# Kernel tuning notes

Hardware: AMD Instinct MI355X
Metric: run time of the kernel (lower is better)

The kernel has to match this reference:

```python
import jax, jax.numpy as jnp
import numpy as np

NEG = -1000000000.0
EPS = 1e-05

def setup_inputs() -> dict:
    key = jax.random.key(0)
    k1, k2, k3, k4, k5 = jax.random.split(key, 5)
    B, L, E, Q = 64, 2048, 512, 256
    encoded_vecs = jax.random.normal(k1, (B, L, E), dtype=jnp.float32)
    query = jax.random.normal(k2, (B, Q), dtype=jnp.float32)
    length = jax.random.randint(k3, (B,), 1, L + 1, dtype=jnp.int32)
    # Xavier-normal-ish params
    W1 = jax.random.normal(k4, (E + Q, E), dtype=jnp.float32) * jnp.sqrt(2.0 / (E + Q + E))
    b1 = jnp.zeros((E,), dtype=jnp.float32)
    v = jax.random.normal(k5, (E,), dtype=jnp.float32) * jnp.sqrt(2.0 / (E + 1))
    return {"encoded_vecs": encoded_vecs, "query": query, "length": length,
            "W1": W1, "b1": b1, "v": v}

def reference(encoded_vecs, query, length, W1, b1, v):
    B, L, E = encoded_vecs.shape
    # broadcast 2D query over the length dim (repeat in torch code)
    q = jnp.broadcast_to(query[:, None, :], (B, L, query.shape[-1]))
    h = jnp.concatenate([encoded_vecs, q], axis=2)            # [B, L, E+Q]
    u = jnp.tanh(jnp.einsum('blc,ce->ble', h, W1) + b1)       # [B, L, E]
    logits = jnp.einsum('ble,e->bl', u, v)                    # [B, L]
    # masked softmax (faithful to masked_softmax in source)
    mask = (jnp.arange(L)[None, :] < length[:, None])         # [B, L] bool
    masked_logits = jnp.where(mask, logits, NEG)
    max_logits = jnp.max(masked_logits, axis=1, keepdims=True)
    exps = jnp.exp(masked_logits - max_logits) * mask.astype(logits.dtype)
    attention = exps / (jnp.sum(exps, axis=1, keepdims=True) + EPS)  # [B, L]
    context = jnp.einsum('bl,ble->be', attention, encoded_vecs)      # [B, E]
    return (context, attention)
```

## Files before the change

### kernel.cpp

```cpp
#include <hip/hip_runtime.h>

typedef __attribute__((ext_vector_type(4))) float float4v;
typedef __attribute__((ext_vector_type(2))) float float2v;
typedef __attribute__((ext_vector_type(8))) short short8;
typedef __attribute__((ext_vector_type(4))) float f32x4;
typedef __attribute__((ext_vector_type(4))) int int4v;

#define NEGV (-1000000000.0f)

#define MTOT (64 * 2048)

__device__ __forceinline__ unsigned short f2bf(float f) {
    unsigned int u = __float_as_uint(f);
    u += 0x7fffu + ((u >> 16) & 1u);
    return (unsigned short)(u >> 16);
}

__device__ __forceinline__ void gload_lds16(const void* g, void* l) {
    __builtin_amdgcn_global_load_lds(
        (__attribute__((address_space(1))) unsigned int*)(unsigned long long)(g),
        (__attribute__((address_space(3))) unsigned int*)(unsigned int)(unsigned long long)(l),
        16, 0, 0);
}

__global__ __launch_bounds__(256)
void prep_wt_kernel(const float* __restrict__ W1, unsigned short* __restrict__ Wt) {
    __shared__ float t[32][33];
    int bx = blockIdx.x & 15;
    int by = blockIdx.x >> 4;
    int tx = threadIdx.x & 31;
    int ty = threadIdx.x >> 5;
    #pragma unroll
    for (int i = 0; i < 4; ++i)
        t[ty + 8 * i][tx] = W1[(bx * 32 + ty + 8 * i) * 512 + by * 32 + tx];
    __syncthreads();
    #pragma unroll
    for (int i = 0; i < 4; ++i)
        Wt[(by * 32 + ty + 8 * i) * 512 + bx * 32 + tx] = f2bf(t[tx][ty + 8 * i]);
}

__global__ void prep_qc_kernel(const float* __restrict__ query, const float* __restrict__ W1,
                               const float* __restrict__ b1, float* __restrict__ qc) {
    int b = blockIdx.x;
    int e = threadIdx.x;
    float acc0 = b1[e];
    float acc1 = b1[e + 256];
    const float* w = W1 + 512 * 512;
    #pragma unroll 8
    for (int q = 0; q < 256; ++q) {
        float qv = query[b * 256 + q];
        acc0 += qv * w[q * 512 + e];
        acc1 += qv * w[q * 512 + e + 256];
    }
    qc[b * 512 + e] = acc0;
    qc[b * 512 + e + 256] = acc1;
}

__global__ __launch_bounds__(256, 3)
void gemm_logits_kernel(const float* __restrict__ A,
                        const unsigned short* __restrict__ Wt,
                        const float* __restrict__ qc,
                        const float* __restrict__ v,
                        const int* __restrict__ length,
                        float* __restrict__ part)
{
    int bid = blockIdx.x;
    int x = bid & 7;
    int j = bid >> 3;
    int bm = (j >> 2) * 8 + x;
    int bn = j & 3;
    int b = bm >> 4;
    int l0 = (bm & 15) * 128;
    if (l0 >= length[b]) return;

    __shared__ unsigned short As[3 * 128 * 32];
    __shared__ unsigned short Bs[3 * 128 * 32];

    int tid = threadIdx.x;
    int lane = tid & 63;
    int w = tid >> 6;
    int wm = w >> 1, wn = w & 1;
    long row0 = (long)bm * 128;
    int col0 = bn * 128;

    int ar_r = w * 32 + (lane >> 1);
    int ar_h = lane & 1;
    const char* gAr = (const char*)A + (row0 + ar_r) * 2048 + ar_h * 64;
    int asw = ((ar_r >> 1) & 3) << 4;
    int awr0 = ar_r * 64 + ((ar_h * 32) ^ asw);
    int awr1 = ar_r * 64 + ((ar_h * 32 + 16) ^ asw);

    const char* gB0;
    const char* gB1;
    {
        int off = (w * 2 + 0) * 1024 + lane * 16;
        int r = off >> 6;
        gB0 = (const char*)Wt + (long)(col0 + r) * 1024 + ((off & 63) ^ (((r >> 1) & 3) << 4));
        off = (w * 2 + 1) * 1024 + lane * 16;
        r = off >> 6;
        gB1 = (const char*)Wt + (long)(col0 + r) * 1024 + ((off & 63) ^ (((r >> 1) & 3) << 4));
    }

    int aoff[4], boff[4];
    int kb = 16 * (lane >> 4);
    #pragma unroll
    for (int mi = 0; mi < 4; ++mi) {
        int ar = wm * 64 + (lane & 15) + mi * 16;
        aoff[mi] = ar * 64 + (kb ^ (((ar >> 1) & 3) << 4));
    }
    #pragma unroll
    for (int ni = 0; ni < 4; ++ni) {
        int br = wn * 64 + (lane & 15) + ni * 16;
        boff[ni] = br * 64 + (kb ^ (((br >> 1) & 3) << 4));
    }

    f32x4 acc[4][4] = {};
    float4v P0, P1, P2, P3, Q0, Q1, Q2, Q3;

#define GISSUE(t, R0, R1, R2, R3, sI) do {                                   \
    const char* ga_ = gAr + (t) * 128;                                       \
    R0 = *(const float4v*)(ga_);                                             \
    R1 = *(const float4v*)(ga_ + 16);                                        \
    R2 = *(const float4v*)(ga_ + 32);                                        \
    R3 = *(const float4v*)(ga_ + 48);                                        \
    char* lb_ = (char*)Bs + (sI) * 8192 + w * 2048;                          \
    gload_lds16(gB0 + (t) * 64, lb_);                                        \
    gload_lds16(gB1 + (t) * 64, lb_ + 1024);                                 \
} while (0)

#define CVTW(R0, R1, R2, R3, sW) do {                                        \
    union { int4v i; short8 s; } u0_, u1_;                                   \
    asm("v_cvt_pk_bf16_f32 %0, %1, %2" : "=v"(u0_.i.x) : "v"(R0[0]), "v"(R0[1])); \
    asm("v_cvt_pk_bf16_f32 %0, %1, %2" : "=v"(u0_.i.y) : "v"(R0[2]), "v"(R0[3])); \
    asm("v_cvt_pk_bf16_f32 %0, %1, %2" : "=v"(u0_.i.z) : "v"(R1[0]), "v"(R1[1])); \
    asm("v_cvt_pk_bf16_f32 %0, %1, %2" : "=v"(u0_.i.w) : "v"(R1[2]), "v"(R1[3])); \
    asm("v_cvt_pk_bf16_f32 %0, %1, %2" : "=v"(u1_.i.x) : "v"(R2[0]), "v"(R2[1])); \
    asm("v_cvt_pk_bf16_f32 %0, %1, %2" : "=v"(u1_.i.y) : "v"(R2[2]), "v"(R2[3])); \
    asm("v_cvt_pk_bf16_f32 %0, %1, %2" : "=v"(u1_.i.z) : "v"(R3[0]), "v"(R3[1])); \
    asm("v_cvt_pk_bf16_f32 %0, %1, %2" : "=v"(u1_.i.w) : "v"(R3[2]), "v"(R3[3])); \
    char* aw_ = (char*)As + (sW) * 8192;                                     \
    *(short8*)(aw_ + awr0) = u0_.s;                                          \
    *(short8*)(aw_ + awr1) = u1_.s;                                          \
} while (0)

#define KCOMP(sC) do {                                                       \
    const char* as_ = (const char*)As + (sC) * 8192;                         \
    const char* bs_ = (const char*)Bs + (sC) * 8192;                         \
    short8 af_[4], bf_[4];                                                   \
    _Pragma("unroll")                                                        \
    for (int mi = 0; mi < 4; ++mi) af_[mi] = *(const short8*)(as_ + aoff[mi]); \
    _Pragma("unroll")                                                        \
    for (int ni = 0; ni < 4; ++ni) bf_[ni] = *(const short8*)(bs_ + boff[ni]); \
    _Pragma("unroll")                                                        \
    for (int mi = 0; mi < 4; ++mi)                                           \
        _Pragma("unroll")                                                    \
        for (int ni = 0; ni < 4; ++ni)                                       \
            acc[mi][ni] = __builtin_amdgcn_mfma_f32_16x16x32_bf16(af_[mi], bf_[ni], acc[mi][ni], 0, 0, 0); \
} while (0)

#define KITER(t, L0, L1, L2, L3, C0, C1, C2, C3, sC, sW, sI, ISS, VM) do {   \
    if (ISS) GISSUE((t) + 2, L0, L1, L2, L3, sI);                            \
    KCOMP(sC);                                                               \
    asm volatile("s_waitcnt vmcnt(" #VM ")" ::: "memory");                   \
    CVTW(C0, C1, C2, C3, sW);                                                \
    asm volatile("s_waitcnt lgkmcnt(0)" ::: "memory");                       \
    __builtin_amdgcn_s_barrier();                                            \
    asm volatile("" ::: "memory");                                           \
} while (0)

    GISSUE(0, P0, P1, P2, P3, 0);
    GISSUE(1, Q0, Q1, Q2, Q3, 1);
    asm volatile("s_waitcnt vmcnt(6)" ::: "memory");
    CVTW(P0, P1, P2, P3, 0);
    asm volatile("s_waitcnt lgkmcnt(0)" ::: "memory");
    __builtin_amdgcn_s_barrier();
    asm volatile("" ::: "memory");

    KITER(0,  P0,P1,P2,P3, Q0,Q1,Q2,Q3, 0,1,2, 1, 6);
    KITER(1,  Q0,Q1,Q2,Q3, P0,P1,P2,P3, 1,2,0, 1, 6);
    KITER(2,  P0,P1,P2,P3, Q0,Q1,Q2,Q3, 2,0,1, 1, 6);
    KITER(3,  Q0,Q1,Q2,Q3, P0,P1,P2,P3, 0,1,2, 1, 6);
    KITER(4,  P0,P1,P2,P3, Q0,Q1,Q2,Q3, 1,2,0, 1, 6);
    KITER(5,  Q0,Q1,Q2,Q3, P0,P1,P2,P3, 2,0,1, 1, 6);
    KITER(6,  P0,P1,P2,P3, Q0,Q1,Q2,Q3, 0,1,2, 1, 6);
    KITER(7,  Q0,Q1,Q2,Q3, P0,P1,P2,P3, 1,2,0, 1, 6);
    KITER(8,  P0,P1,P2,P3, Q0,Q1,Q2,Q3, 2,0,1, 1, 6);
    KITER(9,  Q0,Q1,Q2,Q3, P0,P1,P2,P3, 0,1,2, 1, 6);
    KITER(10, P0,P1,P2,P3, Q0,Q1,Q2,Q3, 1,2,0, 1, 6);
    KITER(11, Q0,Q1,Q2,Q3, P0,P1,P2,P3, 2,0,1, 1, 6);
    KITER(12, P0,P1,P2,P3, Q0,Q1,Q2,Q3, 0,1,2, 1, 6);
    KITER(13, Q0,Q1,Q2,Q3, P0,P1,P2,P3, 1,2,0, 1, 6);
    KITER(14, P0,P1,P2,P3, Q0,Q1,Q2,Q3, 2,0,1, 0, 0);
    KCOMP(0);

    const float* qcb = qc + b * 512;
    float vcol[4], qcol[4];
    #pragma unroll
    for (int ni = 0; ni < 4; ++ni) {
        int c = col0 + wn * 64 + ni * 16 + (lane & 15);
        vcol[ni] = v[c];
        qcol[ni] = qcb[c];
    }
    float* pslice = part + (bn * 2 + wn) * MTOT + row0;
    int rbase = wm * 64 + 4 * (lane >> 4);
    #pragma unroll
    for (int mi = 0; mi < 4; ++mi) {
        #pragma unroll
        for (int j2 = 0; j2 < 4; ++j2) {
            float s = 0.f;
            #pragma unroll
            for (int ni = 0; ni < 4; ++ni) {
                float xx = acc[mi][ni][j2] + qcol[ni];
                float e2 = __expf(2.0f * xx);
                float tt = 1.0f - 2.0f * __builtin_amdgcn_rcpf(e2 + 1.0f);
                s += tt * vcol[ni];
            }
            s += __shfl_xor(s, 1);
            s += __shfl_xor(s, 2);
            s += __shfl_xor(s, 4);
            s += __shfl_xor(s, 8);
            if ((lane & 15) == 0)
                pslice[rbase + mi * 16 + j2] = s;
        }
    }
}

__global__ void softmax_kernel(const float* __restrict__ part, const int* __restrict__ length,
                               float* __restrict__ att, float* __restrict__ ctx) {
    int b = blockIdx.x;
    int len = length[b];
    int tid = threadIdx.x;
    int lane = tid & 63, wv = tid >> 6;
    const float* p0 = part + b * 2048;
    float* ab = att + b * 2048;

    ctx[b * 512 + tid] = 0.f;
    ctx[b * 512 + 256 + tid] = 0.f;

    float vals[8];
    float mymax = -3.402823466e38f;
    #pragma unroll
    for (int i = 0; i < 8; ++i) {
        int l = tid + i * 256;
        float xv = NEGV;
        if (l < len) {
            xv = 0.f;
            #pragma unroll
            for (int s = 0; s < 8; ++s)
                xv += p0[s * MTOT + l];
        }
        vals[i] = xv;
        mymax = fmaxf(mymax, xv);
    }
    #pragma unroll
    for (int m = 32; m; m >>= 1) mymax = fmaxf(mymax, __shfl_xor(mymax, m));
    __shared__ float sm[4];
    if (lane == 0) sm[wv] = mymax;
    __syncthreads();
    float bmax = fmaxf(fmaxf(sm[0], sm[1]), fmaxf(sm[2], sm[3]));

    float mysum = 0.f;
    #pragma unroll
    for (int i = 0; i < 8; ++i) {
        int l = tid + i * 256;
        float e = (l < len) ? __expf(vals[i] - bmax) : 0.f;
        vals[i] = e;
        mysum += e;
    }
    #pragma unroll
    for (int m = 32; m; m >>= 1) mysum += __shfl_xor(mysum, m);
    __shared__ float ss[4];
    if (lane == 0) ss[wv] = mysum;
    __syncthreads();
    float tot = ss[0] + ss[1] + ss[2] + ss[3];
    float inv = 1.0f / (tot + 1e-5f);
    #pragma unroll
    for (int i = 0; i < 8; ++i) {
        int l = tid + i * 256;
        ab[l] = vals[i] * inv;
    }
}

__global__ void ctx_kernel(const float* __restrict__ att, const float* __restrict__ enc,
                           const int* __restrict__ length, float* __restrict__ ctx) {
    int b = blockIdx.x;
    int lc = blockIdx.y;
    int len = length[b];
    int l0 = lc * 128;
    if (l0 >= len) return;
    int lim = len - l0;
    if (lim > 128) lim = 128;

    int t = threadIdx.x;
    const float* ab = att + b * 2048 + l0;
    const float* eb = enc + ((long)(b * 2048 + l0)) * 512 + t * 2;
    float c0 = 0.f, c1 = 0.f;
    #pragma unroll 4
    for (int l = 0; l < lim; ++l) {
        float a = ab[l];
        float2v e = *(const float2v*)(eb);
        eb += 512;
        c0 += a * e.x;
        c1 += a * e.y;
    }
    atomicAdd(&ctx[b * 512 + 2 * t], c0);
    atomicAdd(&ctx[b * 512 + 2 * t + 1], c1);
}

extern "C" void kernel_launch(void* const* d_in, const int* in_sizes, int n_in,
                              void* d_out, int out_size, void* d_ws, size_t ws_size,
                              hipStream_t stream) {
    const float* enc    = (const float*)d_in[0];
    const float* query  = (const float*)d_in[1];
    const int*   length = (const int*)d_in[2];
    const float* W1     = (const float*)d_in[3];
    const float* b1     = (const float*)d_in[4];
    const float* v      = (const float*)d_in[5];

    float* out = (float*)d_out;
    float* ctx = out;
    float* att = out + 64 * 512;

    char* ws = (char*)d_ws;
    float* part        = (float*)ws;
    float* qc          = (float*)(ws + 8 * MTOT * 4);
    unsigned short* Wt = (unsigned short*)(ws + 8 * MTOT * 4 + 64 * 512 * 4);

    prep_wt_kernel<<<256, 256, 0, stream>>>(W1, Wt);
    prep_qc_kernel<<<64, 256, 0, stream>>>(query, W1, b1, qc);

    gemm_logits_kernel<<<4096, 256, 0, stream>>>(enc, Wt, qc, v, length, part);

    softmax_kernel<<<64, 256, 0, stream>>>(part, length, att, ctx);

    dim3 g3(64, 16);
    ctx_kernel<<<g3, 256, 0, stream>>>(att, enc, length, ctx);
}
```

Baseline: 145.0 us.

## Widen GEMM tile to 128x256 with 512 threads and reduce partial logits in LDS

The logits GEMM now uses 512-thread blocks covering 256 output columns, so each A tile is loaded and converted to bf16 once per two column halves instead of once per four. The pipeline drops from triple to double buffering with a single prefetch stage, which adds full vmcnt(0) waits at every barrier. Per-wave partial logit sums are reduced in shared memory before being written, which cuts the partial buffer from 8 slices to 2 and lightens the softmax read. The tradeoff is less latency hiding, since each step now waits on its loads, and lower occupancy from the larger blocks.

```diff
diff --git a/kernel.cpp b/kernel.cpp
--- a/kernel.cpp
+++ b/kernel.cpp
@@ -56,7 +56,7 @@
     qc[b * 512 + e + 256] = acc1;
 }
 
-__global__ __launch_bounds__(256, 3)
+__global__ __launch_bounds__(512)
 void gemm_logits_kernel(const float* __restrict__ A,
                         const unsigned short* __restrict__ Wt,
                         const float* __restrict__ qc,
@@ -67,38 +67,38 @@
     int bid = blockIdx.x;
     int x = bid & 7;
     int j = bid >> 3;
-    int bm = (j >> 2) * 8 + x;
-    int bn = j & 3;
+    int bm = (j >> 1) * 8 + x;
+    int bn = j & 1;
     int b = bm >> 4;
     int l0 = (bm & 15) * 128;
     if (l0 >= length[b]) return;
 
-    __shared__ unsigned short As[3 * 128 * 32];
-    __shared__ unsigned short Bs[3 * 128 * 32];
+    __shared__ unsigned short As[2 * 128 * 32];
+    __shared__ unsigned short Bs[2 * 256 * 32];
+    __shared__ float lred[128][4];
 
     int tid = threadIdx.x;
     int lane = tid & 63;
     int w = tid >> 6;
-    int wm = w >> 1, wn = w & 1;
+    int wm = w >> 2, wn = w & 3;
     long row0 = (long)bm * 128;
-    int col0 = bn * 128;
-
-    int ar_r = w * 32 + (lane >> 1);
-    int ar_h = lane & 1;
-    const char* gAr = (const char*)A + (row0 + ar_r) * 2048 + ar_h * 64;
-    int asw = ((ar_r >> 1) & 3) << 4;
-    int awr0 = ar_r * 64 + ((ar_h * 32) ^ asw);
-    int awr1 = ar_r * 64 + ((ar_h * 32 + 16) ^ asw);
-
+    int col0 = bn * 256;
+
+    int ar_r = tid >> 2;
+    int ar_q = tid & 3;
+    const char* gAr = (const char*)A + (row0 + ar_r) * 2048 + ar_q * 32;
+    int awr = ar_r * 64 + ((ar_q * 16) ^ (((ar_r >> 1) & 3) << 4));
+
+    int offw = w * 2048 + lane * 16;
     const char* gB0;
     const char* gB1;
     {
-        int off = (w * 2 + 0) * 1024 + lane * 16;
-        int r = off >> 6;
-        gB0 = (const char*)Wt + (long)(col0 + r) * 1024 + ((off & 63) ^ (((r >> 1) & 3) << 4));
-        off = (w * 2 + 1) * 1024 + lane * 16;
-        r = off >> 6;
-        gB1 = (const char*)Wt + (long)(col0 + r) * 1024 + ((off & 63) ^ (((r >> 1) & 3) << 4));
+        int o = offw;
+        int r = o >> 6;
+        gB0 = (const char*)Wt + (long)(col0 + r) * 1024 + ((o & 63) ^ (((r >> 1) & 3) << 4));
+        o = offw + 1024;
+        r = o >> 6;
+        gB1 = (const char*)Wt + (long)(col0 + r) * 1024 + ((o & 63) ^ (((r >> 1) & 3) << 4));
     }
 
     int aoff[4], boff[4];
@@ -115,83 +115,63 @@
     }
 
     f32x4 acc[4][4] = {};
-    float4v P0, P1, P2, P3, Q0, Q1, Q2, Q3;
-
-#define GISSUE(t, R0, R1, R2, R3, sI) do {                                   \
+    float4v P0, P1;
+
+#define GISSUE(t, sI) do {                                                   \
     const char* ga_ = gAr + (t) * 128;                                       \
-    R0 = *(const float4v*)(ga_);                                             \
-    R1 = *(const float4v*)(ga_ + 16);                                        \
-    R2 = *(const float4v*)(ga_ + 32);                                        \
-    R3 = *(const float4v*)(ga_ + 48);                                        \
-    char* lb_ = (char*)Bs + (sI) * 8192 + w * 2048;                          \
+    P0 = *(const float4v*)(ga_);                                             \
+    P1 = *(const float4v*)(ga_ + 16);                                        \
+    char* lb_ = (char*)Bs + (sI) * 16384 + offw;                             \
     gload_lds16(gB0 + (t) * 64, lb_);                                        \
     gload_lds16(gB1 + (t) * 64, lb_ + 1024);                                 \
 } while (0)
 
-#define CVTW(R0, R1, R2, R3, sW) do {                                        \
-    union { int4v i; short8 s; } u0_, u1_;                                   \
-    asm("v_cvt_pk_bf16_f32 %0, %1, %2" : "=v"(u0_.i.x) : "v"(R0[0]), "v"(R0[1])); \
-    asm("v_cvt_pk_bf16_f32 %0, %1, %2" : "=v"(u0_.i.y) : "v"(R0[2]), "v"(R0[3])); \
-    asm("v_cvt_pk_bf16_f32 %0, %1, %2" : "=v"(u0_.i.z) : "v"(R1[0]), "v"(R1[1])); \
-    asm("v_cvt_pk_bf16_f32 %0, %1, %2" : "=v"(u0_.i.w) : "v"(R1[2]), "v"(R1[3])); \
-    asm("v_cvt_pk_bf16_f32 %0, %1, %2" : "=v"(u1_.i.x) : "v"(R2[0]), "v"(R2[1])); \
-    asm("v_cvt_pk_bf16_f32 %0, %1, %2" : "=v"(u1_.i.y) : "v"(R2[2]), "v"(R2[3])); \
-    asm("v_cvt_pk_bf16_f32 %0, %1, %2" : "=v"(u1_.i.z) : "v"(R3[0]), "v"(R3[1])); \
-    asm("v_cvt_pk_bf16_f32 %0, %1, %2" : "=v"(u1_.i.w) : "v"(R3[2]), "v"(R3[3])); \
-    char* aw_ = (char*)As + (sW) * 8192;                                     \
-    *(short8*)(aw_ + awr0) = u0_.s;                                          \
-    *(short8*)(aw_ + awr1) = u1_.s;                                          \
+#define CVTW(sW) do {                                                        \
+    union { int4v i; short8 s; } u_;                                         \
+    asm("v_cvt_pk_bf16_f32 %0, %1, %2" : "=v"(u_.i.x) : "v"(P0[0]), "v"(P0[1])); \
+    asm("v_cvt_pk_bf16_f32 %0, %1, %2" : "=v"(u_.i.y) : "v"(P0[2]), "v"(P0[3])); \
+    asm("v_cvt_pk_bf16_f32 %0, %1, %2" : "=v"(u_.i.z) : "v"(P1[0]), "v"(P1[1])); \
+    asm("v_cvt_pk_bf16_f32 %0, %1, %2" : "=v"(u_.i.w) : "v"(P1[2]), "v"(P1[3])); \
+    *(short8*)((char*)As + (sW) * 8192 + awr) = u_.s;                        \
 } while (0)
 
 #define KCOMP(sC) do {                                                       \
     const char* as_ = (const char*)As + (sC) * 8192;                         \
-    const char* bs_ = (const char*)Bs + (sC) * 8192;                         \
-    short8 af_[4], bf_[4];                                                   \
+    const char* bs_ = (const char*)Bs + (sC) * 16384;                        \
+    short8 af_[4];                                                           \
     _Pragma("unroll")                                                        \
     for (int mi = 0; mi < 4; ++mi) af_[mi] = *(const short8*)(as_ + aoff[mi]); \
     _Pragma("unroll")                                                        \
-    for (int ni = 0; ni < 4; ++ni) bf_[ni] = *(const short8*)(bs_ + boff[ni]); \
-    _Pragma("unroll")                                                        \
-    for (int mi = 0; mi < 4; ++mi)                                           \
+    for (int ni = 0; ni < 4; ++ni) {                                         \
+        short8 bf_ = *(const short8*)(bs_ + boff[ni]);                       \
         _Pragma("unroll")                                                    \
-        for (int ni = 0; ni < 4; ++ni)                                       \
-            acc[mi][ni] = __builtin_amdgcn_mfma_f32_16x16x32_bf16(af_[mi], bf_[ni], acc[mi][ni], 0, 0, 0); \
+        for (int mi = 0; mi < 4; ++mi)                                       \
+            acc[mi][ni] = __builtin_amdgcn_mfma_f32_16x16x32_bf16(af_[mi], bf_, acc[mi][ni], 0, 0, 0); \
+    }                                                                        \
 } while (0)
 
-#define KITER(t, L0, L1, L2, L3, C0, C1, C2, C3, sC, sW, sI, ISS, VM) do {   \
-    if (ISS) GISSUE((t) + 2, L0, L1, L2, L3, sI);                            \
-    KCOMP(sC);                                                               \
-    asm volatile("s_waitcnt vmcnt(" #VM ")" ::: "memory");                   \
-    CVTW(C0, C1, C2, C3, sW);                                                \
-    asm volatile("s_waitcnt lgkmcnt(0)" ::: "memory");                       \
+#define KITER(t) do {                                                        \
+    GISSUE((t) + 1, ((t) + 1) & 1);                                          \
+    KCOMP((t) & 1);                                                          \
+    asm volatile("s_waitcnt vmcnt(2)" ::: "memory");                         \
+    CVTW(((t) + 1) & 1);                                                     \
+    asm volatile("s_waitcnt vmcnt(0) lgkmcnt(0)" ::: "memory");              \
     __builtin_amdgcn_s_barrier();                                            \
     asm volatile("" ::: "memory");                                           \
 } while (0)
 
-    GISSUE(0, P0, P1, P2, P3, 0);
-    GISSUE(1, Q0, Q1, Q2, Q3, 1);
-    asm volatile("s_waitcnt vmcnt(6)" ::: "memory");
-    CVTW(P0, P1, P2, P3, 0);
-    asm volatile("s_waitcnt lgkmcnt(0)" ::: "memory");
+    GISSUE(0, 0);
+    asm volatile("s_waitcnt vmcnt(2)" ::: "memory");
+    CVTW(0);
+    asm volatile("s_waitcnt vmcnt(0) lgkmcnt(0)" ::: "memory");
     __builtin_amdgcn_s_barrier();
     asm volatile("" ::: "memory");
 
-    KITER(0,  P0,P1,P2,P3, Q0,Q1,Q2,Q3, 0,1,2, 1, 6);
-    KITER(1,  Q0,Q1,Q2,Q3, P0,P1,P2,P3, 1,2,0, 1, 6);
-    KITER(2,  P0,P1,P2,P3, Q0,Q1,Q2,Q3, 2,0,1, 1, 6);
-    KITER(3,  Q0,Q1,Q2,Q3, P0,P1,P2,P3, 0,1,2, 1, 6);
-    KITER(4,  P0,P1,P2,P3, Q0,Q1,Q2,Q3, 1,2,0, 1, 6);
-    KITER(5,  Q0,Q1,Q2,Q3, P0,P1,P2,P3, 2,0,1, 1, 6);
-    KITER(6,  P0,P1,P2,P3, Q0,Q1,Q2,Q3, 0,1,2, 1, 6);
-    KITER(7,  Q0,Q1,Q2,Q3, P0,P1,P2,P3, 1,2,0, 1, 6);
-    KITER(8,  P0,P1,P2,P3, Q0,Q1,Q2,Q3, 2,0,1, 1, 6);
-    KITER(9,  Q0,Q1,Q2,Q3, P0,P1,P2,P3, 0,1,2, 1, 6);
-    KITER(10, P0,P1,P2,P3, Q0,Q1,Q2,Q3, 1,2,0, 1, 6);
-    KITER(11, Q0,Q1,Q2,Q3, P0,P1,P2,P3, 2,0,1, 1, 6);
-    KITER(12, P0,P1,P2,P3, Q0,Q1,Q2,Q3, 0,1,2, 1, 6);
-    KITER(13, Q0,Q1,Q2,Q3, P0,P1,P2,P3, 1,2,0, 1, 6);
-    KITER(14, P0,P1,P2,P3, Q0,Q1,Q2,Q3, 2,0,1, 0, 0);
-    KCOMP(0);
+    KITER(0);  KITER(1);  KITER(2);  KITER(3);
+    KITER(4);  KITER(5);  KITER(6);  KITER(7);
+    KITER(8);  KITER(9);  KITER(10); KITER(11);
+    KITER(12); KITER(13); KITER(14);
+    KCOMP(1);
 
     const float* qcb = qc + b * 512;
     float vcol[4], qcol[4];
@@ -201,8 +181,6 @@
         vcol[ni] = v[c];
         qcol[ni] = qcb[c];
     }
-    float* pslice = part + (bn * 2 + wn) * MTOT + row0;
-    int rbase = wm * 64 + 4 * (lane >> 4);
     #pragma unroll
     for (int mi = 0; mi < 4; ++mi) {
         #pragma unroll
@@ -220,8 +198,13 @@
             s += __shfl_xor(s, 4);
             s += __shfl_xor(s, 8);
             if ((lane & 15) == 0)
-                pslice[rbase + mi * 16 + j2] = s;
+                lred[wm * 64 + mi * 16 + 4 * (lane >> 4) + j2][wn] = s;
         }
+    }
+    __syncthreads();
+    if (tid < 128) {
+        float lg = lred[tid][0] + lred[tid][1] + lred[tid][2] + lred[tid][3];
+        part[bn * MTOT + row0 + tid] = lg;
     }
 }
 
@@ -243,12 +226,8 @@
     for (int i = 0; i < 8; ++i) {
         int l = tid + i * 256;
         float xv = NEGV;
-        if (l < len) {
-            xv = 0.f;
-            #pragma unroll
-            for (int s = 0; s < 8; ++s)
-                xv += p0[s * MTOT + l];
-        }
+        if (l < len)
+            xv = p0[l] + p0[MTOT + l];
         vals[i] = xv;
         mymax = fmaxf(mymax, xv);
     }
@@ -323,13 +302,13 @@
 
     char* ws = (char*)d_ws;
     float* part        = (float*)ws;
-    float* qc          = (float*)(ws + 8 * MTOT * 4);
-    unsigned short* Wt = (unsigned short*)(ws + 8 * MTOT * 4 + 64 * 512 * 4);
+    float* qc          = (float*)(ws + 2 * MTOT * 4);
+    unsigned short* Wt = (unsigned short*)(ws + 2 * MTOT * 4 + 64 * 512 * 4);
 
     prep_wt_kernel<<<256, 256, 0, stream>>>(W1, Wt);
     prep_qc_kernel<<<64, 256, 0, stream>>>(query, W1, b1, qc);
 
-    gemm_logits_kernel<<<4096, 256, 0, stream>>>(enc, Wt, qc, v, length, part);
+    gemm_logits_kernel<<<2048, 512, 0, stream>>>(enc, Wt, qc, v, length, part);
 
     softmax_kernel<<<64, 256, 0, stream>>>(part, length, att, ctx);
 
```

After: 173.4 us. 1.2x slower.
